# Optimization experiments

Hardware: AMD Instinct MI355X
Metric: run time of the kernel (lower is better)

The kernel has to match this reference:

```python
import jax, jax.numpy as jnp
import numpy as np

G = 512            # voxel grid extent per axis
B = 2              # batches
N_PER_BATCH = 20000
EPS = 1e-5
SLOPE = 0.01       # LeakyReLU default negative_slope
OFFS = [(dx, dy, dz) for dx in (-1, 0, 1) for dy in (-1, 0, 1) for dz in (-1, 0, 1)]


def _keys(coords, stride):
    # coords: [N,4] int32 (batch,x,y,z), multiples of stride -> unique int32 key
    Gs = G // stride
    c = coords[:, 1:] // stride
    return ((coords[:, 0] * Gs + c[:, 0]) * Gs + c[:, 1]) * Gs + c[:, 2]


def _sorted_keys(in_coords, in_stride):
    keys = _keys(in_coords, in_stride)
    perm = jnp.argsort(keys)
    return keys[perm], perm


def _query(ks, perm, out_coords, off, in_stride):
    # hash-free kernel-map lookup: binary search of neighbor key in sorted keys
    q = out_coords[:, 1:] + jnp.array(off, jnp.int32) * in_stride
    valid = jnp.all((q >= 0) & (q < G), axis=1)
    qc = jnp.clip(q, 0, G - 1) // in_stride
    Gs = G // in_stride
    qk = ((out_coords[:, 0] * Gs + qc[:, 0]) * Gs + qc[:, 1]) * Gs + qc[:, 2]
    pos = jnp.clip(jnp.searchsorted(ks, qk), 0, ks.shape[0] - 1)
    hit = valid & (ks[pos] == qk)
    return jnp.where(hit, perm[pos], 0), hit


def sparse_conv(feats, in_coords, out_coords, W, in_stride):
    # gather-GEMM-scatter sparse conv, kernel 3^3, W: [27, Cin, Cout]
    ks, perm = _sorted_keys(in_coords, in_stride)
    out = jnp.zeros((out_coords.shape[0], W.shape[-1]), feats.dtype)
    for k, off in enumerate(OFFS):
        idx, hit = _query(ks, perm, out_coords, off, in_stride)
        f = jnp.where(hit[:, None], feats[idx], jnp.zeros((), feats.dtype))
        out = out + f @ W[k]
    return out


def sparse_maxpool(feats, in_coords, out_coords, in_stride):
    ks, perm = _sorted_keys(in_coords, in_stride)
    NEG = jnp.asarray(-3.0e38, feats.dtype)
    out = jnp.full((out_coords.shape[0], feats.shape[1]), NEG, feats.dtype)
    for off in OFFS:
        idx, hit = _query(ks, perm, out_coords, off, in_stride)
        out = jnp.maximum(out, jnp.where(hit[:, None], feats[idx], NEG))
    return out


def slice_to_field(level_feats, level_coords, field_coords, stride):
    # TensorField.slice: map coarse sparse features back to every field point
    ks, perm = _sorted_keys(level_coords, stride)
    qk = _keys(field_coords, stride)
    pos = jnp.clip(jnp.searchsorted(ks, qk), 0, ks.shape[0] - 1)
    return level_feats[perm[pos]]


def bn_lrelu(x, gamma, beta):
    # MinkowskiBatchNorm (training-mode batch stats) + LeakyReLU
    mu = x.mean(0)
    var = ((x - mu) ** 2).mean(0)
    y = (x - mu) * jax.lax.rsqrt(var + EPS) * gamma + beta
    return jnp.where(y >= 0, y, SLOPE * y)


def setup_inputs() -> dict:
    rng = np.random.default_rng(0)
    coords_np = []
    for b in range(B):
        lin = np.unique(rng.integers(0, G ** 3, size=2 * N_PER_BATCH, dtype=np.int64))
        rng.shuffle(lin)
        lin = lin[:N_PER_BATCH]
        x, r = lin // (G * G), lin % (G * G)
        coords_np.append(np.stack([np.full(N_PER_BATCH, b, np.int64), x, r // G, r % G], 1))
    coords_np = np.concatenate(coords_np, 0)

    def level(s):
        q = coords_np.copy()
        q[:, 1:] = (q[:, 1:] // s) * s
        key = ((q[:, 0] * G + q[:, 1]) * G + q[:, 2]) * G + q[:, 3]
        uk = np.unique(key)
        b, r = uk // G ** 3, uk % G ** 3
        return np.stack([b, r // (G * G), (r // G) % G, r % G], 1).astype(np.int32)

    levels = {('c%d' % s): jnp.asarray(level(s)) for s in (2, 4, 8, 16, 32, 64, 128)}
    ks = jax.random.split(jax.random.key(0), 9)

    def conv_w(k, cin, cout):
        return jax.random.normal(k, (27, cin, cout), jnp.float32) * np.float32(np.sqrt(2.0 / (27 * cin)))

    inp = dict(
        feats=jax.random.normal(ks[0], (coords_np.shape[0], 1), jnp.float32),
        coords=jnp.asarray(coords_np.astype(np.int32)),
        w_mlp=jax.random.normal(ks[1], (1, 32), jnp.float32),
        gm=jnp.ones(32, jnp.float32), bm=jnp.zeros(32, jnp.float32),
        W1=conv_w(ks[2], 32, 48), g1=jnp.ones(48, jnp.float32), b1=jnp.zeros(48, jnp.float32),
        W2=conv_w(ks[3], 48, 64), g2=jnp.ones(64, jnp.float32), b2=jnp.zeros(64, jnp.float32),
        W3=conv_w(ks[4], 64, 96), g3=jnp.ones(96, jnp.float32), b3=jnp.zeros(96, jnp.float32),
        W4=conv_w(ks[5], 96, 128), g4=jnp.ones(128, jnp.float32), b4=jnp.zeros(128, jnp.float32),
        W5a=conv_w(ks[6], 336, 256), g5a=jnp.ones(256, jnp.float32), b5a=jnp.zeros(256, jnp.float32),
        W5b=conv_w(ks[7], 256, 512), g5b=jnp.ones(512, jnp.float32), b5b=jnp.zeros(512, jnp.float32),
        W5c=conv_w(ks[8], 512, 1024), g5c=jnp.ones(1024, jnp.float32), b5c=jnp.zeros(1024, jnp.float32),
    )
    inp.update(levels)
    return inp


def reference(feats, coords, c2, c4, c8, c16, c32, c64, c128, w_mlp, gm, bm,
              W1, g1, b1, W2, g2, b2, W3, g3, b3, W4, g4, b4,
              W5a, g5a, b5a, W5b, g5b, b5b, W5c, g5c, b5c):
    # mlp1 on the tensor field (coords are unique, so field == sparse tensor)
    x = bn_lrelu(feats @ w_mlp, gm, bm)                            # [N,32]
    y = bn_lrelu(sparse_conv(x, coords, coords, W1, 1), g1, b1)    # stride 1, 48
    y1 = sparse_maxpool(y, coords, c2, 1)                          # stride 2
    y = bn_lrelu(sparse_conv(y1, c2, c4, W2, 2), g2, b2)           # stride 4, 64
    y2 = sparse_maxpool(y, c4, c8, 4)                              # stride 8
    y = bn_lrelu(sparse_conv(y2, c8, c16, W3, 8), g3, b3)          # stride 16, 96
    y3 = sparse_maxpool(y, c16, c32, 16)                           # stride 32
    y = bn_lrelu(sparse_conv(y3, c32, c64, W4, 32), g4, b4)        # stride 64, 128
    y4 = sparse_maxpool(y, c64, c128, 64)                          # stride 128
    x1 = slice_to_field(y1, c2, coords, 2)
    x2 = slice_to_field(y2, c8, coords, 8)
    x3 = slice_to_field(y3, c32, coords, 32)
    x4 = slice_to_field(y4, c128, coords, 128)
    xc = jnp.concatenate([x1, x2, x3, x4], axis=1)                 # [N,336]
    y = bn_lrelu(sparse_conv(xc, coords, c2, W5a, 1), g5a, b5a)    # stride 2, 256
    y = bn_lrelu(sparse_conv(y, c2, c4, W5b, 2), g5b, b5b)         # stride 4, 512
    y = bn_lrelu(sparse_conv(y, c4, c8, W5c, 4), g5c, b5c)         # stride 8, 1024
    return y
```

## Files before the change

### kernel.cpp

```cpp
#include <hip/hip_runtime.h>
#include <cstdint>
#include <cstddef>

#define GDIM 512

typedef __attribute__((ext_vector_type(8))) short short8;
typedef __attribute__((ext_vector_type(4))) float f32x4;
typedef __attribute__((ext_vector_type(4))) unsigned short ushort4v;

__device__ __forceinline__ short f2bf(float f) {
  unsigned u = __float_as_uint(f);
  u = u + 0x7fffu + ((u >> 16) & 1u);
  return (short)(u >> 16);
}

__device__ __forceinline__ int hash_lookup(int key, const int* __restrict__ keys,
                                           const int* __restrict__ vals, unsigned capmask) {
  unsigned slot = ((unsigned)key * 2654435761u) & capmask;
  while (true) {
    int kk = keys[slot];
    if (kk == key) return vals[slot];
    if (kk == -1) return -1;
    slot = (slot + 1) & capmask;
  }
}

__global__ void k_build_table(const int* __restrict__ coords, int n, int sh, int Gs,
                              int* __restrict__ keys, int* __restrict__ vals, unsigned capmask) {
  int i = blockIdx.x * blockDim.x + threadIdx.x;
  if (i >= n) return;
  int b = coords[4 * i];
  int key = ((b * Gs + (coords[4 * i + 1] >> sh)) * Gs + (coords[4 * i + 2] >> sh)) * Gs +
            (coords[4 * i + 3] >> sh);
  unsigned slot = ((unsigned)key * 2654435761u) & capmask;
  while (true) {
    int prev = atomicCAS(&keys[slot], -1, key);
    if (prev == -1) { vals[slot] = i; return; }
    slot = (slot + 1) & capmask;
  }
}

__global__ void k_query_idx_t(const int* __restrict__ oc, int m, int sh, int Gs,
                              const int* __restrict__ keys, const int* __restrict__ vals,
                              unsigned capmask, int* __restrict__ idxT) {
  int k = blockIdx.y;
  int o = blockIdx.x * blockDim.x + threadIdx.x;
  if (o >= m) return;
  int stride = 1 << sh;
  int dx = k / 9 - 1, dy = (k / 3) % 3 - 1, dz = k % 3 - 1;
  int4 c = *(const int4*)(oc + 4 * o);
  int qx = c.y + dx * stride;
  int qy = c.z + dy * stride;
  int qz = c.w + dz * stride;
  int res = -1;
  if ((unsigned)qx < GDIM && (unsigned)qy < GDIM && (unsigned)qz < GDIM) {
    int key = ((c.x * Gs + (qx >> sh)) * Gs + (qy >> sh)) * Gs + (qz >> sh);
    res = hash_lookup(key, keys, vals, capmask);
  }
  idxT[(size_t)k * m + o] = res;
}

__global__ void k_make_pairs(const int* __restrict__ idxT, int m,
                             int* __restrict__ po_o, int* __restrict__ pi_o,
                             int* __restrict__ po_r, int* __restrict__ pi_r,
                             int* __restrict__ cnts, int mcap) {
  int o = blockIdx.x * blockDim.x + threadIdx.x;
  bool act = o < m;
  int lane = threadIdx.x & 63;
  bool owned = false;
  for (int k = 0; k < 27; ++k) {
    int i = act ? idxT[(size_t)k * m + o] : -1;
    bool hit = i >= 0;
    bool isown = hit && !owned;
    if (isown) owned = true;
    bool isrest = hit && !isown;
    unsigned long long bo = __ballot(isown);
    if (bo) {
      int ldr = __ffsll((unsigned long long)bo) - 1;
      int base = 0;
      if (lane == ldr) base = atomicAdd(&cnts[k], __popcll(bo));
      base = __shfl(base, ldr);
      if (isown) {
        int p = base + __popcll(bo & ((1ull << lane) - 1ull));
        po_o[k * mcap + p] = o;
        pi_o[k * mcap + p] = i;
      }
    }
    unsigned long long br = __ballot(isrest);
    if (br) {
      int ldr = __ffsll((unsigned long long)br) - 1;
      int base = 0;
      if (lane == ldr) base = atomicAdd(&cnts[27 + k], __popcll(br));
      base = __shfl(base, ldr);
      if (isrest) {
        int p = base + __popcll(br & ((1ull << lane) - 1ull));
        po_r[k * mcap + p] = o;
        pi_r[k * mcap + p] = i;
      }
    }
  }
}

__global__ void k_plan(const int* __restrict__ cnts, int* __restrict__ plan) {
  if (threadIdx.x == 0) {
    int acc = 0;
    for (int k = 0; k < 27; ++k) { plan[k] = acc; acc += (cnts[k] + 127) >> 7; }
    plan[27] = acc;
    acc = 0;
    for (int k = 0; k < 27; ++k) { plan[28 + k] = acc; acc += (cnts[27 + k] + 127) >> 7; }
    plan[55] = acc;
  }
}

template<bool OWNER>
__global__ __launch_bounds__(256) void k_conv_mfma(
    const unsigned short* __restrict__ Fb,
    const short* __restrict__ Wt,
    float* __restrict__ out,
    const int* __restrict__ plo, const int* __restrict__ pli,
    const int* __restrict__ counts, const int* __restrict__ plan,
    int cin, int cin_pad, int cout, int mcap) {
  __shared__ int pshared[28];
  __shared__ short Alds[128 * 72];
  __shared__ short Blds[2][128 * 40];
  __shared__ int rows_out[128];
  __shared__ int rows_in[128];

  int tid = threadIdx.x;
  if (tid < 28) pshared[tid] = plan[tid];
  __syncthreads();
  int NB = pshared[27];

  int n0 = blockIdx.x << 7;
  int wave = tid >> 6, lane = tid & 63;
  int wm = (wave & 1) * 64, wn = (wave >> 1) * 64;
  int lm = lane & 15, quad = lane >> 4;
  int bn0 = tid >> 2, bk0 = (tid & 3) << 3;
  int bn1 = (tid + 256) >> 2, bk1 = ((tid + 256) & 3) << 3;
  int S = cin_pad >> 5;

  for (int v = blockIdx.y; v < NB; v += gridDim.y) {
    int k = 0;
    #pragma unroll
    for (int kk = 1; kk < 27; ++kk) k += (v >= pshared[kk]);
    int cnt = counts[k];
    int p0 = (v - pshared[k]) << 7;
    int np = min(128, cnt - p0);

    __syncthreads();
    if (tid < 128) {
      rows_out[tid] = (tid < np) ? plo[k * mcap + p0 + tid] : -1;
      rows_in [tid] = (tid < np) ? pli[k * mcap + p0 + tid] : -1;
    }
    const short* Wk = Wt + (size_t)k * cout * cin;
    f32x4 acc[4][4] = {};

    short8 br0 = {0, 0, 0, 0, 0, 0, 0, 0}, br1 = br0;
    {
      int gn = n0 + bn0;
      if (gn < cout && bk0 < cin) br0 = *(const short8*)(Wk + (size_t)gn * cin + bk0);
      gn = n0 + bn1;
      if (gn < cout && bk1 < cin) br1 = *(const short8*)(Wk + (size_t)gn * cin + bk1);
    }
    for (int s = 0; s < S; ++s) {
      int ks = s << 5;
      __syncthreads();
      if ((s & 1) == 0) {
        int kslab = min(64, cin_pad - ks);
        int clog = (kslab == 64) ? 3 : 2;
        for (int u = tid; u < (128 << clog); u += 256) {
          int r = u >> clog;
          int kc = (u - (r << clog)) << 3;
          int gk = ks + kc;
          int irow = rows_in[r];
          short8 v8 = {0, 0, 0, 0, 0, 0, 0, 0};
          if (irow >= 0 && gk < cin)
            v8 = *(const short8*)((const short*)Fb + (size_t)irow * cin + gk);
          *(short8*)(Alds + r * 72 + kc) = v8;
        }
      }
      *(short8*)(&Blds[s & 1][bn0 * 40 + bk0]) = br0;
      *(short8*)(&Blds[s & 1][bn1 * 40 + bk1]) = br1;
      if (s + 1 < S) {
        int gkb = (s + 1) << 5;
        short8 z = {0, 0, 0, 0, 0, 0, 0, 0};
        br0 = z; br1 = z;
        int gn = n0 + bn0, gk = gkb + bk0;
        if (gn < cout && gk < cin) br0 = *(const short8*)(Wk + (size_t)gn * cin + gk);
        gn = n0 + bn1; gk = gkb + bk1;
        if (gn < cout && gk < cin) br1 = *(const short8*)(Wk + (size_t)gn * cin + gk);
      }
      __syncthreads();
      int ka = ((s & 1) << 5) + quad * 8;
      short8 a[4], b[4];
      #pragma unroll
      for (int mt = 0; mt < 4; ++mt)
        a[mt] = *(const short8*)(Alds + (wm + mt * 16 + lm) * 72 + ka);
      #pragma unroll
      for (int nt = 0; nt < 4; ++nt)
        b[nt] = *(const short8*)(&Blds[s & 1][(wn + nt * 16 + lm) * 40 + quad * 8]);
      #pragma unroll
      for (int mt = 0; mt < 4; ++mt)
        #pragma unroll
        for (int nt = 0; nt < 4; ++nt)
          acc[mt][nt] = __builtin_amdgcn_mfma_f32_16x16x32_bf16(a[mt], b[nt], acc[mt][nt], 0, 0, 0);
    }
    #pragma unroll
    for (int mt = 0; mt < 4; ++mt)
      #pragma unroll
      for (int nt = 0; nt < 4; ++nt)
        #pragma unroll
        for (int r = 0; r < 4; ++r) {
          int row = wm + mt * 16 + quad * 4 + r;
          int col = n0 + wn + nt * 16 + lm;
          if (row < np && col < cout) {
            if (OWNER)
              out[(size_t)rows_out[row] * cout + col] = acc[mt][nt][r];
            else
              atomicAdd(&out[(size_t)rows_out[row] * cout + col], acc[mt][nt][r]);
          }
        }
  }
}

__global__ void k_convert_w(const float* __restrict__ W, short* __restrict__ Wt,
                            int cin, int cout) {
  __shared__ float tile[32][33];
  int k = blockIdx.z;
  int n0 = blockIdx.x * 32, c0 = blockIdx.y * 32;
  int tx = threadIdx.x & 31, ty = threadIdx.x >> 5;
  const float* Wk = W + (size_t)k * cin * cout;
  for (int i = ty; i < 32; i += 8) {
    int c = c0 + i, n = n0 + tx;
    tile[i][tx] = (c < cin && n < cout) ? Wk[(size_t)c * cout + n] : 0.f;
  }
  __syncthreads();
  short* Wtk = Wt + (size_t)k * cout * cin;
  for (int i = ty; i < 32; i += 8) {
    int n = n0 + i, c = c0 + tx;
    if (n < cout && c < cin) Wtk[(size_t)n * cin + c] = f2bf(tile[tx][i]);
  }
}

__global__ void k_query_idx(const int* __restrict__ oc, int m, int sh, int Gs,
                            const int* __restrict__ keys, const int* __restrict__ vals,
                            unsigned capmask, int* __restrict__ idx) {
  int t = blockIdx.x * blockDim.x + threadIdx.x;
  if (t >= m * 27) return;
  int o = t / 27, k = t - o * 27;
  int stride = 1 << sh;
  int dx = k / 9 - 1, dy = (k / 3) % 3 - 1, dz = k % 3 - 1;
  int b  = oc[4 * o];
  int qx = oc[4 * o + 1] + dx * stride;
  int qy = oc[4 * o + 2] + dy * stride;
  int qz = oc[4 * o + 3] + dz * stride;
  int res = -1;
  if ((unsigned)qx < GDIM && (unsigned)qy < GDIM && (unsigned)qz < GDIM) {
    int key = ((b * Gs + (qx >> sh)) * Gs + (qy >> sh)) * Gs + (qz >> sh);
    res = hash_lookup(key, keys, vals, capmask);
  }
  idx[t] = res;
}

__global__ void k_maxpool_bn(const float* __restrict__ F, unsigned short* __restrict__ out,
                             const int* __restrict__ idx, int m, int C,
                             const float* __restrict__ ab) {
  long long t = (long long)blockIdx.x * blockDim.x + threadIdx.x;
  if (t >= (long long)m * C) return;
  int o = (int)(t / C), c = (int)(t - (long long)o * C);
  float a = ab[c], b = ab[C + c];
  float best = -3e38f;
  #pragma unroll 1
  for (int k = 0; k < 27; ++k) {
    int i = idx[o * 27 + k];
    if (i >= 0) {
      float y = a * F[(size_t)i * C + c] + b;
      y = fmaxf(y, 0.01f * y);
      best = fmaxf(best, y);
    }
  }
  out[t] = (unsigned short)f2bf(best);
}

__global__ void k_slice_idx(const int* __restrict__ coords, int n, int sh, int Gs,
                            const int* __restrict__ keys, const int* __restrict__ vals,
                            unsigned capmask, int* __restrict__ sidx) {
  int i = blockIdx.x * blockDim.x + threadIdx.x;
  if (i >= n) return;
  int b = coords[4 * i];
  int key = ((b * Gs + (coords[4 * i + 1] >> sh)) * Gs + (coords[4 * i + 2] >> sh)) * Gs +
            (coords[4 * i + 3] >> sh);
  int v = hash_lookup(key, keys, vals, capmask);
  sidx[i] = (v < 0) ? 0 : v;
}

__global__ void k_gather_cols16(const unsigned short* __restrict__ src, int C,
                                const int* __restrict__ sidx,
                                unsigned short* __restrict__ dst, int dstC, int colOff, int n) {
  long long t = (long long)blockIdx.x * blockDim.x + threadIdx.x;
  if (t >= (long long)n * C) return;
  int o = (int)(t / C), c = (int)(t - (long long)o * C);
  dst[(size_t)o * dstC + colOff + c] = src[(size_t)sidx[o] * C + c];
}

__global__ void k_mlp(const float* __restrict__ feats, const float* __restrict__ w,
                      float* __restrict__ x, int n) {
  int t = blockIdx.x * blockDim.x + threadIdx.x;
  if (t >= n * 32) return;
  x[t] = feats[t >> 5] * w[t & 31];
}

__global__ void k_bn_stats(const float* __restrict__ x, int m, int C,
                           float* __restrict__ sums) {
  __shared__ float ls[2][256];
  int tid = threadIdx.x;
  int RL = (C >= 256) ? 1 : (256 / C);
  int c, rl;
  bool active;
  if (C >= 256) { c = blockIdx.y * 256 + tid; rl = 0; active = true; }
  else { c = tid % C; rl = tid / C; active = (tid < RL * C); }
  float s = 0.f, s2 = 0.f;
  if (active) {
    int step = gridDim.x * RL;
    for (int r = blockIdx.x * RL + rl; r < m; r += step) {
      float v = x[(size_t)r * C + c];
      s += v; s2 += v * v;
    }
  }
  if (RL == 1) {
    atomicAdd(&sums[c], s);
    atomicAdd(&sums[C + c], s2);
  } else {
    ls[0][tid] = s; ls[1][tid] = s2;
    __syncthreads();
    if (tid < C) {
      for (int j = 1; j < RL; ++j) { s += ls[0][c + j * C]; s2 += ls[1][c + j * C]; }
      atomicAdd(&sums[c], s);
      atomicAdd(&sums[C + c], s2);
    }
  }
}

__global__ void k_bn_finalize(const float* __restrict__ sums, const float* __restrict__ gamma,
                              const float* __restrict__ beta, int C, float inv_m,
                              float* __restrict__ ab) {
  for (int c = threadIdx.x; c < C; c += 256) {
    float mu  = sums[c] * inv_m;
    float var = sums[C + c] * inv_m - mu * mu;
    float a = rsqrtf(var + 1e-5f) * gamma[c];
    ab[c] = a;
    ab[C + c] = beta[c] - mu * a;
  }
}

__global__ void k_bn_bf16(const float* __restrict__ x, unsigned short* __restrict__ xb,
                          long long total4, int C, const float* __restrict__ ab) {
  long long t = (long long)blockIdx.x * blockDim.x + threadIdx.x;
  if (t >= total4) return;
  long long e = t * 4;
  int c = (int)(e % C);
  float4 v = *(const float4*)(x + e);
  ushort4v o;
  float y0 = ab[c] * v.x + ab[C + c];         o.x = (unsigned short)f2bf(fmaxf(y0, 0.01f * y0));
  float y1 = ab[c + 1] * v.y + ab[C + c + 1]; o.y = (unsigned short)f2bf(fmaxf(y1, 0.01f * y1));
  float y2 = ab[c + 2] * v.z + ab[C + c + 2]; o.z = (unsigned short)f2bf(fmaxf(y2, 0.01f * y2));
  float y3 = ab[c + 3] * v.w + ab[C + c + 3]; o.w = (unsigned short)f2bf(fmaxf(y3, 0.01f * y3));
  *(ushort4v*)(xb + e) = o;
}

__global__ void k_bn_apply(float* __restrict__ x, long long total4, int C,
                           const float* __restrict__ ab) {
  long long t = (long long)blockIdx.x * blockDim.x + threadIdx.x;
  if (t >= total4) return;
  long long e = t * 4;
  int c = (int)(e % C);
  float4 v = *(const float4*)(x + e);
  float y0 = ab[c] * v.x + ab[C + c];         v.x = fmaxf(y0, 0.01f * y0);
  float y1 = ab[c + 1] * v.y + ab[C + c + 1]; v.y = fmaxf(y1, 0.01f * y1);
  float y2 = ab[c + 2] * v.z + ab[C + c + 2]; v.z = fmaxf(y2, 0.01f * y2);
  float y3 = ab[c + 3] * v.w + ab[C + c + 3]; v.w = fmaxf(y3, 0.01f * y3);
  *(float4*)(x + e) = v;
}

static inline int cdiv(int a, int b) { return (a + b - 1) / b; }

extern "C" void kernel_launch(void* const* d_in, const int* in_sizes, int n_in,
                              void* d_out, int out_size, void* d_ws, size_t ws_size,
                              hipStream_t stream) {
  (void)n_in; (void)out_size; (void)ws_size;
  const float* feats  = (const float*)d_in[0];
  const int*   coords = (const int*)d_in[1];
  const float* w_mlp = (const float*)d_in[2];
  const float* gm  = (const float*)d_in[3];  const float* bm  = (const float*)d_in[4];
  const float* W1  = (const float*)d_in[5];  const float* g1  = (const float*)d_in[6];  const float* b1  = (const float*)d_in[7];
  const float* W2  = (const float*)d_in[8];  const float* g2  = (const float*)d_in[9];  const float* b2  = (const float*)d_in[10];
  const float* W3  = (const float*)d_in[11]; const float* g3  = (const float*)d_in[12]; const float* b3  = (const float*)d_in[13];
  const float* W4  = (const float*)d_in[14]; const float* g4  = (const float*)d_in[15]; const float* b4  = (const float*)d_in[16];
  const float* W5a = (const float*)d_in[17]; const float* g5a = (const float*)d_in[18]; const float* b5a = (const float*)d_in[19];
  const float* W5b = (const float*)d_in[20]; const float* g5b = (const float*)d_in[21]; const float* b5b = (const float*)d_in[22];
  const float* W5c = (const float*)d_in[23]; const float* g5c = (const float*)d_in[24]; const float* b5c = (const float*)d_in[25];
  const int*   lvl[7];
  for (int i = 0; i < 7; ++i) lvl[i] = (const int*)d_in[26 + i];

  const int N = in_sizes[0];
  int nl[7];
  for (int i = 0; i < 7; ++i) nl[i] = in_sizes[26 + i] / 4;
  const int n2 = nl[0], n4 = nl[1], n8 = nl[2], n16 = nl[3], n32 = nl[4], n64 = nl[5], n128 = nl[6];

  char* ws = (char*)d_ws;
  size_t off = 0;
  auto alloc = [&](size_t bytes) -> char* {
    off = (off + 255) & ~(size_t)255;
    char* p = ws + off;
    off += bytes;
    return p;
  };

  struct Tab { int* keys; int* vals; unsigned mask; int sh; int Gs; int n; const int* src; };
  Tab tab[8];
  const int* tsrc[8] = {coords, lvl[0], lvl[1], lvl[2], lvl[3], lvl[4], lvl[5], lvl[6]};
  int tn[8] = {N, n2, n4, n8, n16, n32, n64, n128};
  for (int i = 0; i < 8; ++i) {
    int cap = 64;
    while (cap < 2 * tn[i]) cap <<= 1;
    tab[i].keys = (int*)alloc((size_t)cap * 4);
    tab[i].vals = (int*)alloc((size_t)cap * 4);
    tab[i].mask = (unsigned)(cap - 1);
    tab[i].sh = i;
    tab[i].Gs = GDIM >> i;
    tab[i].n = tn[i];
    tab[i].src = tsrc[i];
  }

  int* pout   = (int*)alloc((size_t)27 * N * 4);
  int* pin    = (int*)alloc((size_t)27 * N * 4);
  int* pout_r = (int*)alloc((size_t)27 * N * 4);
  int* pin_r  = (int*)alloc((size_t)27 * N * 4);
  int* counts = (int*)alloc(256);
  int* plan   = (int*)alloc(256);
  int* idxbuf = (int*)alloc((size_t)27 * N * 4);
  int* sidx[4];
  for (int i = 0; i < 4; ++i) sidx[i] = (int*)alloc((size_t)N * 4);
  float* bnsum = (float*)alloc(2 * 1024 * 4);
  float* abuf  = (float*)alloc(2 * 1024 * 4);

  auto mxz = [](size_t a, size_t b) { return a > b ? a : b; };
  size_t szA = mxz(mxz((size_t)N * 32, (size_t)n4 * 64), (size_t)n64 * 128) * 4;
  size_t szB = mxz(mxz((size_t)N * 48, (size_t)n16 * 96), (size_t)n2 * 256) * 4;
  float* RA = (float*)alloc(szA);
  float* RB = (float*)alloc(szB);
  float* RG = (float*)alloc((size_t)n4 * 512 * 4);
  unsigned short* xb  = (unsigned short*)alloc((size_t)N * 32 * 2);
  unsigned short* y1b = (unsigned short*)alloc((size_t)n2 * 48 * 2);
  unsigned short* y2b = (unsigned short*)alloc((size_t)n8 * 64 * 2);
  unsigned short* y3b = (unsigned short*)alloc((size_t)n32 * 96 * 2);
  unsigned short* y4b = (unsigned short*)alloc((size_t)n128 * 128 * 2);
  unsigned short* xcb = (unsigned short*)alloc((size_t)N * 336 * 2);
  unsigned short* t5bb = (unsigned short*)alloc((size_t)n4 * 512 * 2);
  short* Wt1  = (short*)alloc((size_t)27 * 32 * 48 * 2);
  short* Wt2  = (short*)alloc((size_t)27 * 48 * 64 * 2);
  short* Wt3  = (short*)alloc((size_t)27 * 64 * 96 * 2);
  short* Wt4  = (short*)alloc((size_t)27 * 96 * 128 * 2);
  short* Wt5a = (short*)alloc((size_t)27 * 336 * 256 * 2);
  short* Wt5b = (short*)alloc((size_t)27 * 256 * 512 * 2);
  short* Wt5c = (short*)alloc((size_t)27 * 512 * 1024 * 2);

  for (int i = 0; i < 8; ++i)
    hipMemsetAsync(tab[i].keys, 0xFF, (size_t)(tab[i].mask + 1) * 4, stream);
  for (int i = 0; i < 8; ++i)
    k_build_table<<<cdiv(tab[i].n, 256), 256, 0, stream>>>(
        tab[i].src, tab[i].n, tab[i].sh, tab[i].Gs, tab[i].keys, tab[i].vals, tab[i].mask);

  auto convW = [&](const float* W, short* Wt, int cin, int cout) {
    dim3 g(cdiv(cout, 32), cdiv(cin, 32), 27);
    k_convert_w<<<g, 256, 0, stream>>>(W, Wt, cin, cout);
  };
  convW(W1, Wt1, 32, 48);     convW(W2, Wt2, 48, 64);
  convW(W3, Wt3, 64, 96);     convW(W4, Wt4, 96, 128);
  convW(W5a, Wt5a, 336, 256); convW(W5b, Wt5b, 256, 512);
  convW(W5c, Wt5c, 512, 1024);

  auto conv = [&](const unsigned short* Fb, const short* Wt, const int* oc, int m,
                  const Tab& t, int cin, int cout, float* out) {
    hipMemsetAsync(counts, 0, 54 * 4, stream);
    dim3 gq(cdiv(m, 256), 27);
    k_query_idx_t<<<gq, 256, 0, stream>>>(oc, m, t.sh, t.Gs, t.keys, t.vals, t.mask, idxbuf);
    k_make_pairs<<<cdiv(m, 256), 256, 0, stream>>>(idxbuf, m, pout, pin, pout_r, pin_r,
                                                   counts, N);
    k_plan<<<1, 64, 0, stream>>>(counts, plan);
    int cin_pad = (cin + 31) & ~31;
    int nT = cdiv(cout, 128);
    int GY = cdiv(m, 128) + 27;
    if (GY > 2048) GY = 2048;
    dim3 gridc(nT, GY);
    k_conv_mfma<true><<<gridc, 256, 0, stream>>>(Fb, Wt, out, pout, pin, counts, plan,
                                                 cin, cin_pad, cout, N);
    k_conv_mfma<false><<<gridc, 256, 0, stream>>>(Fb, Wt, out, pout_r, pin_r, counts + 27,
                                                  plan + 28, cin, cin_pad, cout, N);
  };
  auto stats = [&](const float* x, int m, int C, const float* gamma, const float* beta) {
    hipMemsetAsync(bnsum, 0, (size_t)2 * C * 4, stream);
    int CG = (C >= 256) ? (C / 256) : 1;
    int RL = (C >= 256) ? 1 : (256 / C);
    int NS = (C >= 256) ? 512 : 256;
    int maxNS = cdiv(m, RL);
    if (NS > maxNS) NS = maxNS < 1 ? 1 : maxNS;
    dim3 g(NS, CG);
    k_bn_stats<<<g, 256, 0, stream>>>(x, m, C, bnsum);
    k_bn_finalize<<<1, 256, 0, stream>>>(bnsum, gamma, beta, C, 1.0f / (float)m, abuf);
  };
  auto pool = [&](const float* F, const int* oc, int m, const Tab& t, int C,
                  unsigned short* out) {
    k_query_idx<<<cdiv(m * 27, 256), 256, 0, stream>>>(
        oc, m, t.sh, t.Gs, t.keys, t.vals, t.mask, idxbuf);
    long long total = (long long)m * C;
    k_maxpool_bn<<<(int)((total + 255) / 256), 256, 0, stream>>>(F, out, idxbuf, m, C, abuf);
  };
  auto cvt = [&](const float* src, unsigned short* dst, long long total, int C) {
    long long t4 = total / 4;
    k_bn_bf16<<<(int)((t4 + 255) / 256), 256, 0, stream>>>(src, dst, t4, C, abuf);
  };

  float* x = RA;
  k_mlp<<<cdiv(N * 32, 256), 256, 0, stream>>>(feats, w_mlp, x, N);
  stats(x, N, 32, gm, bm);
  cvt(x, xb, (long long)N * 32, 32);

  float* t1 = RB;
  conv(xb, Wt1, coords, N, tab[0], 32, 48, t1);
  stats(t1, N, 48, g1, b1);
  pool(t1, lvl[0], n2, tab[0], 48, y1b);

  float* t2 = RA;
  conv(y1b, Wt2, lvl[1], n4, tab[1], 48, 64, t2);
  stats(t2, n4, 64, g2, b2);
  pool(t2, lvl[2], n8, tab[2], 64, y2b);

  float* t3 = RB;
  conv(y2b, Wt3, lvl[3], n16, tab[3], 64, 96, t3);
  stats(t3, n16, 96, g3, b3);
  pool(t3, lvl[4], n32, tab[4], 96, y3b);

  float* t4 = RA;
  conv(y3b, Wt4, lvl[5], n64, tab[5], 96, 128, t4);
  stats(t4, n64, 128, g4, b4);
  pool(t4, lvl[6], n128, tab[6], 128, y4b);

  k_slice_idx<<<cdiv(N, 256), 256, 0, stream>>>(coords, N, tab[1].sh, tab[1].Gs,
                                                tab[1].keys, tab[1].vals, tab[1].mask, sidx[0]);
  k_slice_idx<<<cdiv(N, 256), 256, 0, stream>>>(coords, N, tab[3].sh, tab[3].Gs,
                                                tab[3].keys, tab[3].vals, tab[3].mask, sidx[1]);
  k_slice_idx<<<cdiv(N, 256), 256, 0, stream>>>(coords, N, tab[5].sh, tab[5].Gs,
                                                tab[5].keys, tab[5].vals, tab[5].mask, sidx[2]);
  k_slice_idx<<<cdiv(N, 256), 256, 0, stream>>>(coords, N, tab[7].sh, tab[7].Gs,
                                                tab[7].keys, tab[7].vals, tab[7].mask, sidx[3]);
  k_gather_cols16<<<(int)(((long long)N * 48 + 255) / 256), 256, 0, stream>>>(y1b, 48, sidx[0], xcb, 336, 0, N);
  k_gather_cols16<<<(int)(((long long)N * 64 + 255) / 256), 256, 0, stream>>>(y2b, 64, sidx[1], xcb, 336, 48, N);
  k_gather_cols16<<<(int)(((long long)N * 96 + 255) / 256), 256, 0, stream>>>(y3b, 96, sidx[2], xcb, 336, 112, N);
  k_gather_cols16<<<(int)(((long long)N * 128 + 255) / 256), 256, 0, stream>>>(y4b, 128, sidx[3], xcb, 336, 208, N);

  float* t5a = RB;
  conv(xcb, Wt5a, lvl[0], n2, tab[0], 336, 256, t5a);
  stats(t5a, n2, 256, g5a, b5a);
  unsigned short* t5ab = xcb;
  cvt(t5a, t5ab, (long long)n2 * 256, 256);

  float* t5b = RG;
  conv(t5ab, Wt5b, lvl[1], n4, tab[1], 256, 512, t5b);
  stats(t5b, n4, 512, g5b, b5b);
  cvt(t5b, t5bb, (long long)n4 * 512, 512);

  float* outp = (float*)d_out;
  conv(t5bb, Wt5c, lvl[2], n8, tab[2], 512, 1024, outp);
  stats(outp, n8, 1024, g5c, b5c);
  long long total4 = (long long)n8 * 1024 / 4;
  k_bn_apply<<<(int)((total4 + 255) / 256), 256, 0, stream>>>(outp, total4, 1024, abuf);
}
```

Before: 1.820 ms.

## Parallelize pair building over offsets and double-buffer A tiles via register prefetch

Pair construction is split so the query kernel records each output's first-hit offset with atomicMin, and a new scatter kernel runs over a grid of outputs by 27 offsets instead of looping serially over offsets per thread. The conv kernel now stages both the gathered feature rows and the weights in double-buffered 32-wide LDS tiles (padded stride 44), prefetching the next slab into registers while the current one is computed. This replaces the old scheme that loaded 64-wide A slabs synchronously every other step. The cost is an extra memset and atomics per conv, plus more register use for the prefetch.

```diff
diff --git a/kernel.cpp b/kernel.cpp
--- a/kernel.cpp
+++ b/kernel.cpp
@@ -42,7 +42,8 @@
 
 __global__ void k_query_idx_t(const int* __restrict__ oc, int m, int sh, int Gs,
                               const int* __restrict__ keys, const int* __restrict__ vals,
-                              unsigned capmask, int* __restrict__ idxT) {
+                              unsigned capmask, int* __restrict__ idxT,
+                              int* __restrict__ ownerk) {
   int k = blockIdx.y;
   int o = blockIdx.x * blockDim.x + threadIdx.x;
   if (o >= m) return;
@@ -58,45 +59,43 @@
     res = hash_lookup(key, keys, vals, capmask);
   }
   idxT[(size_t)k * m + o] = res;
-}
-
-__global__ void k_make_pairs(const int* __restrict__ idxT, int m,
-                             int* __restrict__ po_o, int* __restrict__ pi_o,
-                             int* __restrict__ po_r, int* __restrict__ pi_r,
-                             int* __restrict__ cnts, int mcap) {
+  if (res >= 0) atomicMin(&ownerk[o], k);
+}
+
+__global__ void k_scatter_pairs(const int* __restrict__ idxT, const int* __restrict__ ownerk,
+                                int m,
+                                int* __restrict__ po_o, int* __restrict__ pi_o,
+                                int* __restrict__ po_r, int* __restrict__ pi_r,
+                                int* __restrict__ cnts, int mcap) {
+  int k = blockIdx.y;
   int o = blockIdx.x * blockDim.x + threadIdx.x;
-  bool act = o < m;
+  int i = (o < m) ? idxT[(size_t)k * m + o] : -1;
+  bool hit = i >= 0;
+  bool isown = hit && (ownerk[o] == k);
+  bool isrest = hit && !isown;
   int lane = threadIdx.x & 63;
-  bool owned = false;
-  for (int k = 0; k < 27; ++k) {
-    int i = act ? idxT[(size_t)k * m + o] : -1;
-    bool hit = i >= 0;
-    bool isown = hit && !owned;
-    if (isown) owned = true;
-    bool isrest = hit && !isown;
-    unsigned long long bo = __ballot(isown);
-    if (bo) {
-      int ldr = __ffsll((unsigned long long)bo) - 1;
-      int base = 0;
-      if (lane == ldr) base = atomicAdd(&cnts[k], __popcll(bo));
-      base = __shfl(base, ldr);
-      if (isown) {
-        int p = base + __popcll(bo & ((1ull << lane) - 1ull));
-        po_o[k * mcap + p] = o;
-        pi_o[k * mcap + p] = i;
-      }
-    }
-    unsigned long long br = __ballot(isrest);
-    if (br) {
-      int ldr = __ffsll((unsigned long long)br) - 1;
-      int base = 0;
-      if (lane == ldr) base = atomicAdd(&cnts[27 + k], __popcll(br));
-      base = __shfl(base, ldr);
-      if (isrest) {
-        int p = base + __popcll(br & ((1ull << lane) - 1ull));
-        po_r[k * mcap + p] = o;
-        pi_r[k * mcap + p] = i;
-      }
+  unsigned long long bo = __ballot(isown);
+  if (bo) {
+    int ldr = __ffsll((unsigned long long)bo) - 1;
+    int base = 0;
+    if (lane == ldr) base = atomicAdd(&cnts[k], __popcll(bo));
+    base = __shfl(base, ldr);
+    if (isown) {
+      int p = base + __popcll(bo & ((1ull << lane) - 1ull));
+      po_o[k * mcap + p] = o;
+      pi_o[k * mcap + p] = i;
+    }
+  }
+  unsigned long long br = __ballot(isrest);
+  if (br) {
+    int ldr = __ffsll((unsigned long long)br) - 1;
+    int base = 0;
+    if (lane == ldr) base = atomicAdd(&cnts[27 + k], __popcll(br));
+    base = __shfl(base, ldr);
+    if (isrest) {
+      int p = base + __popcll(br & ((1ull << lane) - 1ull));
+      po_r[k * mcap + p] = o;
+      pi_r[k * mcap + p] = i;
     }
   }
 }
@@ -121,8 +120,8 @@
     const int* __restrict__ counts, const int* __restrict__ plan,
     int cin, int cin_pad, int cout, int mcap) {
   __shared__ int pshared[28];
-  __shared__ short Alds[128 * 72];
-  __shared__ short Blds[2][128 * 40];
+  __shared__ short Alds[2][128 * 44];
+  __shared__ short Blds[2][128 * 44];
   __shared__ int rows_out[128];
   __shared__ int rows_in[128];
 
@@ -135,9 +134,10 @@
   int wave = tid >> 6, lane = tid & 63;
   int wm = (wave & 1) * 64, wn = (wave >> 1) * 64;
   int lm = lane & 15, quad = lane >> 4;
-  int bn0 = tid >> 2, bk0 = (tid & 3) << 3;
-  int bn1 = (tid + 256) >> 2, bk1 = ((tid + 256) & 3) << 3;
+  int ar0 = tid >> 2, ak0 = (tid & 3) << 3;
+  int ar1 = ar0 + 64;
   int S = cin_pad >> 5;
+  const short* Fs = (const short*)Fb;
 
   for (int v = blockIdx.y; v < NB; v += gridDim.y) {
     int k = 0;
@@ -152,53 +152,47 @@
       rows_out[tid] = (tid < np) ? plo[k * mcap + p0 + tid] : -1;
       rows_in [tid] = (tid < np) ? pli[k * mcap + p0 + tid] : -1;
     }
+    __syncthreads();
     const short* Wk = Wt + (size_t)k * cout * cin;
     f32x4 acc[4][4] = {};
 
-    short8 br0 = {0, 0, 0, 0, 0, 0, 0, 0}, br1 = br0;
+    short8 pa0 = {0,0,0,0,0,0,0,0}, pa1 = pa0, pb0 = pa0, pb1 = pa0;
     {
-      int gn = n0 + bn0;
-      if (gn < cout && bk0 < cin) br0 = *(const short8*)(Wk + (size_t)gn * cin + bk0);
-      gn = n0 + bn1;
-      if (gn < cout && bk1 < cin) br1 = *(const short8*)(Wk + (size_t)gn * cin + bk1);
+      int i0 = rows_in[ar0], i1 = rows_in[ar1];
+      if (i0 >= 0 && ak0 < cin) pa0 = *(const short8*)(Fs + (size_t)i0 * cin + ak0);
+      if (i1 >= 0 && ak0 < cin) pa1 = *(const short8*)(Fs + (size_t)i1 * cin + ak0);
+      int gn0 = n0 + ar0, gn1 = n0 + ar1;
+      if (gn0 < cout && ak0 < cin) pb0 = *(const short8*)(Wk + (size_t)gn0 * cin + ak0);
+      if (gn1 < cout && ak0 < cin) pb1 = *(const short8*)(Wk + (size_t)gn1 * cin + ak0);
     }
     for (int s = 0; s < S; ++s) {
-      int ks = s << 5;
       __syncthreads();
-      if ((s & 1) == 0) {
-        int kslab = min(64, cin_pad - ks);
-        int clog = (kslab == 64) ? 3 : 2;
-        for (int u = tid; u < (128 << clog); u += 256) {
-          int r = u >> clog;
-          int kc = (u - (r << clog)) << 3;
-          int gk = ks + kc;
-          int irow = rows_in[r];
-          short8 v8 = {0, 0, 0, 0, 0, 0, 0, 0};
-          if (irow >= 0 && gk < cin)
-            v8 = *(const short8*)((const short*)Fb + (size_t)irow * cin + gk);
-          *(short8*)(Alds + r * 72 + kc) = v8;
-        }
-      }
-      *(short8*)(&Blds[s & 1][bn0 * 40 + bk0]) = br0;
-      *(short8*)(&Blds[s & 1][bn1 * 40 + bk1]) = br1;
+      short* A = Alds[s & 1];
+      short* B = Blds[s & 1];
+      *(short8*)(A + ar0 * 44 + ak0) = pa0;
+      *(short8*)(A + ar1 * 44 + ak0) = pa1;
+      *(short8*)(B + ar0 * 44 + ak0) = pb0;
+      *(short8*)(B + ar1 * 44 + ak0) = pb1;
       if (s + 1 < S) {
-        int gkb = (s + 1) << 5;
-        short8 z = {0, 0, 0, 0, 0, 0, 0, 0};
-        br0 = z; br1 = z;
-        int gn = n0 + bn0, gk = gkb + bk0;
-        if (gn < cout && gk < cin) br0 = *(const short8*)(Wk + (size_t)gn * cin + gk);
-        gn = n0 + bn1; gk = gkb + bk1;
-        if (gn < cout && gk < cin) br1 = *(const short8*)(Wk + (size_t)gn * cin + gk);
+        int gk = ((s + 1) << 5) + ak0;
+        short8 z = {0,0,0,0,0,0,0,0};
+        pa0 = z; pa1 = z; pb0 = z; pb1 = z;
+        int i0 = rows_in[ar0], i1 = rows_in[ar1];
+        if (i0 >= 0 && gk < cin) pa0 = *(const short8*)(Fs + (size_t)i0 * cin + gk);
+        if (i1 >= 0 && gk < cin) pa1 = *(const short8*)(Fs + (size_t)i1 * cin + gk);
+        int gn0 = n0 + ar0, gn1 = n0 + ar1;
+        if (gn0 < cout && gk < cin) pb0 = *(const short8*)(Wk + (size_t)gn0 * cin + gk);
+        if (gn1 < cout && gk < cin) pb1 = *(const short8*)(Wk + (size_t)gn1 * cin + gk);
       }
       __syncthreads();
-      int ka = ((s & 1) << 5) + quad * 8;
+      int ka = quad * 8;
       short8 a[4], b[4];
       #pragma unroll
       for (int mt = 0; mt < 4; ++mt)
-        a[mt] = *(const short8*)(Alds + (wm + mt * 16 + lm) * 72 + ka);
+        a[mt] = *(const short8*)(A + (wm + mt * 16 + lm) * 44 + ka);
       #pragma unroll
       for (int nt = 0; nt < 4; ++nt)
-        b[nt] = *(const short8*)(&Blds[s & 1][(wn + nt * 16 + lm) * 40 + quad * 8]);
+        b[nt] = *(const short8*)(B + (wn + nt * 16 + lm) * 44 + ka);
       #pragma unroll
       for (int mt = 0; mt < 4; ++mt)
         #pragma unroll
@@ -439,6 +433,7 @@
   int* counts = (int*)alloc(256);
   int* plan   = (int*)alloc(256);
   int* idxbuf = (int*)alloc((size_t)27 * N * 4);
+  int* ownerk = (int*)alloc((size_t)N * 4);
   int* sidx[4];
   for (int i = 0; i < 4; ++i) sidx[i] = (int*)alloc((size_t)N * 4);
   float* bnsum = (float*)alloc(2 * 1024 * 4);
@@ -483,10 +478,12 @@
   auto conv = [&](const unsigned short* Fb, const short* Wt, const int* oc, int m,
                   const Tab& t, int cin, int cout, float* out) {
     hipMemsetAsync(counts, 0, 54 * 4, stream);
+    hipMemsetAsync(ownerk, 0x7F, (size_t)m * 4, stream);
     dim3 gq(cdiv(m, 256), 27);
-    k_query_idx_t<<<gq, 256, 0, stream>>>(oc, m, t.sh, t.Gs, t.keys, t.vals, t.mask, idxbuf);
-    k_make_pairs<<<cdiv(m, 256), 256, 0, stream>>>(idxbuf, m, pout, pin, pout_r, pin_r,
-                                                   counts, N);
+    k_query_idx_t<<<gq, 256, 0, stream>>>(oc, m, t.sh, t.Gs, t.keys, t.vals, t.mask,
+                                          idxbuf, ownerk);
+    k_scatter_pairs<<<gq, 256, 0, stream>>>(idxbuf, ownerk, m, pout, pin, pout_r, pin_r,
+                                            counts, N);
     k_plan<<<1, 64, 0, stream>>>(counts, plan);
     int cin_pad = (cin + 31) & ~31;
     int nT = cdiv(cout, 128);
```

After: 2.096 ms. 1.15x slower.
